# Kernel optimization log

Hardware: AMD Instinct MI355X
Metric: run time of the kernel (lower is better)

Reference implementation:

```python
import jax, jax.numpy as jnp
import numpy as np

EPS = 1e-9
KERNEL = 3


def kernel_tile(x, kernel, stride):
    """im2col-style patch extraction. x: [B,H,W,...] -> [B,OH,OW,kernel*kernel,depth]."""
    B, H, W = x.shape[:3]
    depth = int(np.prod(x.shape[3:]))
    x = x.reshape(B, H, W, depth)
    OH = (H - kernel) // stride + 1
    OW = (W - kernel) // stride + 1
    patches = jnp.stack(
        [x[:, i:i + (OH - 1) * stride + 1:stride, j:j + (OW - 1) * stride + 1:stride, :]
         for i in range(kernel) for j in range(kernel)], axis=3)
    return patches  # [B,OH,OW,k*k,depth]


def em_routing(votes, i_act, beta_v, beta_a, routings):
    # votes: [B,S,S,I,O,16], i_act: [B,S,S,I], beta_*: [1,1,1,O]
    I, O = votes.shape[-3], votes.shape[-2]
    rr = jnp.full((I, O, 1), 1.0 / O, dtype=votes.dtype)
    i_act = i_act[..., None, None]           # [B,S,S,I,1,1]
    bv = beta_v[..., None, :, None]          # [1,1,1,1,O,1]
    ba = beta_a[..., None, :, None]
    it_min, it_max = 1.0, min(float(routings), 3.0)
    o_mean = o_act = None
    for it in range(routings):
        inv_temp = it_min + (it_max - it_min) * it / max(1.0, routings - 1.0)
        # M-step
        rr_prime = rr * i_act                                        # [B,S,S,I,O,1]
        rr_sum = jnp.sum(rr_prime, axis=-3, keepdims=True)           # [B,S,S,1,O,1]
        o_mean = jnp.sum(rr_prime * votes, axis=-3, keepdims=True) / rr_sum  # [B,S,S,1,O,16]
        o_stdv = jnp.sqrt(jnp.sum(rr_prime * jnp.square(votes - o_mean), axis=-3, keepdims=True) / rr_sum)
        o_cost = (bv + jnp.log(o_stdv + EPS)) * rr_sum               # [B,S,S,1,O,16]
        o_act = jax.nn.sigmoid(inv_temp * (ba - jnp.sum(o_cost, axis=-1, keepdims=True)))  # [B,S,S,1,O,1]
        if it < routings - 1:
            # E-step: log Gaussian prob of each vote under each output capsule
            o_p = (-jnp.sum(jnp.square(votes - o_mean) / (2.0 * jnp.square(o_stdv)), axis=-1, keepdims=True)
                   - jnp.sum(jnp.log(o_stdv + EPS), axis=-1, keepdims=True))  # [B,S,S,I,O,1]
            zz = jnp.log(o_act + EPS) + o_p
            rr = jax.nn.softmax(zz, axis=-2)                          # softmax over O
    pose = jnp.squeeze(o_mean, axis=-3)      # [B,S,S,O,16]
    act = jnp.squeeze(o_act, axis=(-3, -1))  # [B,S,S,O]
    return pose, act


def setup_inputs() -> dict:
    key = jax.random.key(0)
    ks = jax.random.split(key, 5)
    B, H, W, I_SIZE, O_SIZE = 4, 14, 14, 32, 32
    inputs_pose = jax.random.normal(ks[0], (B, H, W, I_SIZE, 4, 4), dtype=jnp.float32)
    inputs_activation = jax.random.uniform(ks[1], (B, H, W, I_SIZE), dtype=jnp.float32)
    w = jax.random.normal(ks[2], (1, 3 * 3 * I_SIZE, O_SIZE, 4, 4), dtype=jnp.float32)
    beta_v = 0.1 * jax.random.normal(ks[3], (1, 1, 1, O_SIZE), dtype=jnp.float32)
    beta_a = 0.1 * jax.random.normal(ks[4], (1, 1, 1, O_SIZE), dtype=jnp.float32)
    return {"inputs_pose": inputs_pose, "inputs_activation": inputs_activation,
            "w": w, "beta_v": beta_v, "beta_a": beta_a, "stride": 1, "routings": 3}


def reference(inputs_pose, inputs_activation, w, beta_v, beta_a, stride, routings):
    B = inputs_pose.shape[0]
    pose_size = inputs_pose.shape[-1]            # 4
    i_size = inputs_pose.shape[3]
    o_size = w.shape[2]
    tp = kernel_tile(inputs_pose, KERNEL, stride)        # [B,S,S,9,i*16]
    ta = kernel_tile(inputs_activation, KERNEL, stride)  # [B,S,S,9,i]
    S = ta.shape[1]
    I = KERNEL * KERNEL * i_size
    poses = tp.reshape(-1, I, pose_size, pose_size)      # [N,I,4,4], N = B*S*S
    acts = ta.reshape(B, S, S, I)
    # vote transform: per (input capsule, output capsule) 4x4 matmul
    votes = jnp.einsum('nipq,ioqr->niopr', poses, w[0])  # [N,I,O,4,4]
    votes = votes.reshape(B, S, S, I, o_size, pose_size * pose_size)
    pose, activation = em_routing(votes, acts, beta_v, beta_a, routings)
    pose = pose.reshape(B, S, S, o_size, pose_size, pose_size)
    return pose, activation
```

## Files before the change

### kernel.cpp

```cpp
#include <hip/hip_runtime.h>
#include <math.h>

namespace {

constexpr int SOUT = 12;
constexpr int OCAP = 32;
constexpr int PD   = 16;
constexpr int NI   = 288;
constexpr int SUBS = 4;
constexpr int ISUB = NI / SUBS;
constexpr int NPOS = 4 * SOUT * SOUT;
constexpr float EPSF = 1e-9f;
constexpr int CHUNK = 33 * 32;
constexpr size_t POSE_OUT = (size_t)NPOS * OCAP * PD;

typedef float v2f __attribute__((ext_vector_type(2)));

__device__ __forceinline__ v2f vfma(v2f a, v2f b, v2f c) { return __builtin_elementwise_fma(a, b, c); }
__device__ __forceinline__ v2f splat(float a) { v2f r; r.x = a; r.y = a; return r; }

template<int CTRL>
__device__ __forceinline__ float dppf(float x) {
    return __int_as_float(__builtin_amdgcn_update_dpp(0, __float_as_int(x), CTRL, 0xF, 0xF, true));
}
#define SWZ16(x) __int_as_float(__builtin_amdgcn_ds_swizzle(__float_as_int(x), (16 << 10) | 0x1F))

__device__ __forceinline__ float redmax32(float x) {
    x = fmaxf(x, dppf<0xB1>(x));
    x = fmaxf(x, dppf<0x4E>(x));
    x = fmaxf(x, dppf<0x141>(x));
    x = fmaxf(x, dppf<0x140>(x));
    x = fmaxf(x, SWZ16(x));
    return x;
}
__device__ __forceinline__ float redsum32(float x) {
    x += dppf<0xB1>(x);
    x += dppf<0x4E>(x);
    x += dppf<0x141>(x);
    x += dppf<0x140>(x);
    x += SWZ16(x);
    return x;
}

__device__ __forceinline__ void loadW(const float* __restrict__ p, v2f (&W)[8]) {
    const float4 w0 = *reinterpret_cast<const float4*>(p);
    const float4 w1 = *reinterpret_cast<const float4*>(p + 4);
    const float4 w2 = *reinterpret_cast<const float4*>(p + 8);
    const float4 w3 = *reinterpret_cast<const float4*>(p + 12);
    W[0].x=w0.x; W[0].y=w0.y; W[1].x=w0.z; W[1].y=w0.w;
    W[2].x=w1.x; W[2].y=w1.y; W[3].x=w1.z; W[3].y=w1.w;
    W[4].x=w2.x; W[4].y=w2.y; W[5].x=w2.z; W[5].y=w2.w;
    W[6].x=w3.x; W[6].y=w3.y; W[7].x=w3.z; W[7].y=w3.w;
}

__device__ __forceinline__ void vote8(const float* __restrict__ pr, const v2f (&W)[8], v2f (&v)[8]) {
    #pragma unroll
    for (int p = 0; p < 4; ++p) {
        const float4 pv = *reinterpret_cast<const float4*>(pr + p * 4);
        #pragma unroll
        for (int h = 0; h < 2; ++h) {
            v2f acc = splat(pv.w) * W[6 + h];
            acc = vfma(splat(pv.z), W[4 + h], acc);
            acc = vfma(splat(pv.y), W[2 + h], acc);
            acc = vfma(splat(pv.x), W[0 + h], acc);
            v[p * 2 + h] = acc;
        }
    }
}

__device__ __forceinline__ constexpr int DH(int h) { return (h >> 1) * 4 + (h & 1) * 2; }

template<int SWEEP>
__global__ __launch_bounds__(256, 2)
void sweep_kernel(const float* __restrict__ pose_in,
                  const float* __restrict__ act_in,
                  const float* __restrict__ wmat,
                  const float* __restrict__ beta_v,
                  const float* __restrict__ beta_a,
                  const float* __restrict__ prev,
                  float* __restrict__ outbuf)
{
    __shared__ __align__(16) float sP[ISUB * PD];
    __shared__ float sA[ISUB];
    __shared__ __align__(8) float sStat[OCAP][2 * PD + 2];
    __shared__ float sBias[OCAP];
    __shared__ float sRed[2][33][33];

    const int bid = blockIdx.x;
    const int n   = bid >> 2;
    const int sub = bid & 3;
    const int b   = n / (SOUT * SOUT);
    const int yx  = n % (SOUT * SOUT);
    const int y   = yx / SOUT;
    const int x   = yx % SOUT;

    const int t    = threadIdx.x;
    const int wave = t >> 6;
    const int o    = t & 31;
    const int slot = t >> 5;
    const int half = slot & 1;

    {
        const float4* src = reinterpret_cast<const float4*>(pose_in);
        float4* dst = reinterpret_cast<float4*>(sP);
        for (int u = t; u < ISUB * 4; u += 256) {
            const int il = u >> 2;
            const int i  = sub * ISUB + il;
            const int k = i >> 5, c = i & 31;
            const int ki = k / 3, kj = k - ki * 3;
            const int cell = (b * 14 + y + ki) * 14 + (x + kj);
            dst[u] = src[(size_t)(cell * 32 + c) * 4 + (u & 3)];
        }
        if (t < ISUB) {
            const int i = sub * ISUB + t;
            const int k = i >> 5, c = i & 31;
            const int ki = k / 3, kj = k - ki * 3;
            const int cell = (b * 14 + y + ki) * 14 + (x + kj);
            sA[t] = act_in[(size_t)cell * 32 + c];
        }
    }

    if constexpr (SWEEP > 0) {
        const int oo = t >> 3, dp = t & 7, d0 = dp * 2;
        const float* base = prev + (size_t)n * (SUBS * CHUNK);
        float s0 = 0.f, S1a = 0.f, S1b = 0.f, S2a = 0.f, S2b = 0.f;
        #pragma unroll
        for (int s = 0; s < SUBS; ++s) {
            const float* c = base + s * CHUNK;
            s0  += c[32 * 32 + oo];
            S1a += c[(d0)      * 32 + oo];
            S1b += c[(d0 + 1)  * 32 + oo];
            S2a += c[(16 + d0) * 32 + oo];
            S2b += c[(17 + d0) * 32 + oo];
        }
        const float inv = 1.f / s0;
        const float m0 = S1a * inv, m1 = S1b * inv;
        const float v0 = fmaxf(fmaf(-m0, m0, S2a * inv), 0.f);
        const float v1 = fmaxf(fmaf(-m1, m1, S2b * inv), 0.f);
        const float i20 = 0.5f / fmaxf(v0, 1e-30f);
        const float i21 = 0.5f / fmaxf(v1, 1e-30f);
        float ll = __logf(sqrtf(v0) + EPSF) + __logf(sqrtf(v1) + EPSF);
        float c0 = m0 * m0 * i20 + m1 * m1 * i21;
        sStat[oo][d0]          = i20;
        sStat[oo][d0 + 1]      = i21;
        sStat[oo][16 + d0]     = -2.f * m0 * i20;
        sStat[oo][17 + d0]     = -2.f * m1 * i21;
        #pragma unroll
        for (int m = 1; m <= 4; m <<= 1) {
            ll += __shfl_xor(ll, m, 8);
            c0 += __shfl_xor(c0, m, 8);
        }
        if (dp == 0) {
            const float cost = s0 * fmaf(16.f, beta_v[oo], ll);
            const float oact = 1.f / (1.f + __expf(-(float)SWEEP * (beta_a[oo] - cost)));
            sBias[oo] = __logf(oact + EPSF) - ll - c0;
        }
    }
    __syncthreads();

    float bias_r = 0.f;
    v2f i2r[8], ngr[8];
    if constexpr (SWEEP > 0) {
        bias_r = sBias[o];
        #pragma unroll
        for (int h = 0; h < 8; ++h) {
            i2r[h] = *reinterpret_cast<const v2f*>(&sStat[o][2 * h]);
            ngr[h] = *reinterpret_cast<const v2f*>(&sStat[o][16 + 2 * h]);
        }
    }

    v2f s1[8], s2[8];
    float s0acc = 0.f;
    #pragma unroll
    for (int h = 0; h < 8; ++h) { s1[h] = splat(0.f); s2[h] = splat(0.f); }

    const float* wbase = wmat + ((size_t)(sub * ISUB + slot) * OCAP + o) * PD;

    v2f WA[8], WB[8];
    loadW(wbase, WA);

#define STEP(st, Wc, Wn)                                                   \
    {                                                                      \
        if ((st) < 8) loadW(wbase + (size_t)((st) + 1) * 4096, Wn);        \
        const int il = (st) * 8 + slot;                                    \
        v2f v[8];                                                          \
        vote8(&sP[il * PD], Wc, v);                                        \
        const float a_i = sA[il];                                          \
        float rrp;                                                         \
        if constexpr (SWEEP == 0) {                                        \
            rrp = a_i * (1.0f / 32.0f);                                    \
        } else {                                                           \
            v2f ts2 = splat(0.f);                                          \
            _Pragma("unroll")                                              \
            for (int h = 0; h < 8; ++h) {                                  \
                const v2f tmp = vfma(v[h], i2r[h], ngr[h]);                \
                ts2 = vfma(v[h], tmp, ts2);                                \
            }                                                              \
            const float zz = bias_r - (ts2.x + ts2.y);                     \
            const float m = redmax32(zz);                                  \
            const float e = __expf(zz - m);                                \
            const float es = redsum32(e);                                  \
            rrp = __fdividef(e, es) * a_i;                                 \
        }                                                                  \
        s0acc += rrp;                                                      \
        const v2f rr2 = splat(rrp);                                        \
        _Pragma("unroll")                                                  \
        for (int h = 0; h < 8; ++h) {                                      \
            const v2f rv = rr2 * v[h];                                     \
            s1[h] = s1[h] + rv;                                            \
            s2[h] = vfma(rv, v[h], s2[h]);                                 \
        }                                                                  \
    }

    STEP(0, WA, WB); STEP(1, WB, WA); STEP(2, WA, WB); STEP(3, WB, WA);
    STEP(4, WA, WB); STEP(5, WB, WA); STEP(6, WA, WB); STEP(7, WB, WA);
    STEP(8, WA, WB);
#undef STEP

    #pragma unroll
    for (int h = 0; h < 8; ++h) {
        s1[h].x += __shfl_xor(s1[h].x, 32, 64);
        s1[h].y += __shfl_xor(s1[h].y, 32, 64);
        s2[h].x += __shfl_xor(s2[h].x, 32, 64);
        s2[h].y += __shfl_xor(s2[h].y, 32, 64);
    }
    s0acc += __shfl_xor(s0acc, 32, 64);

    if (wave < 2 && half == 0) {
        #pragma unroll
        for (int h = 0; h < 8; ++h) {
            sRed[wave][DH(h)][o]          = s1[h].x;
            sRed[wave][DH(h) + 1][o]      = s1[h].y;
            sRed[wave][16 + DH(h)][o]     = s2[h].x;
            sRed[wave][16 + DH(h) + 1][o] = s2[h].y;
        }
        sRed[wave][32][o] = s0acc;
    }
    __syncthreads();
    if (wave >= 2 && half == 0) {
        #pragma unroll
        for (int h = 0; h < 8; ++h) {
            sRed[wave - 2][DH(h)][o]          += s1[h].x;
            sRed[wave - 2][DH(h) + 1][o]      += s1[h].y;
            sRed[wave - 2][16 + DH(h)][o]     += s2[h].x;
            sRed[wave - 2][16 + DH(h) + 1][o] += s2[h].y;
        }
        sRed[wave - 2][32][o] += s0acc;
    }
    __syncthreads();

    float* dstc = outbuf + (size_t)bid * CHUNK;
    const int oc = t & 31;
    for (int j = t >> 5; j < 33; j += 8)
        dstc[j * 32 + oc] = sRed[0][j][oc] + sRed[1][j][oc];
}

__global__ __launch_bounds__(256, 4)
void final_kernel(const float* __restrict__ prev,
                  const float* __restrict__ beta_v,
                  const float* __restrict__ beta_a,
                  float* __restrict__ out)
{
    const int n  = blockIdx.x;
    const int t  = threadIdx.x;
    const int oo = t >> 3, dp = t & 7, d0 = dp * 2;
    const float* base = prev + (size_t)n * (SUBS * CHUNK);
    float s0 = 0.f, S1a = 0.f, S1b = 0.f, S2a = 0.f, S2b = 0.f;
    #pragma unroll
    for (int s = 0; s < SUBS; ++s) {
        const float* c = base + s * CHUNK;
        s0  += c[32 * 32 + oo];
        S1a += c[(d0)      * 32 + oo];
        S1b += c[(d0 + 1)  * 32 + oo];
        S2a += c[(16 + d0) * 32 + oo];
        S2b += c[(17 + d0) * 32 + oo];
    }
    const float inv = 1.f / s0;
    const float m0 = S1a * inv, m1 = S1b * inv;
    out[(size_t)n * (OCAP * PD) + oo * PD + d0]     = m0;
    out[(size_t)n * (OCAP * PD) + oo * PD + d0 + 1] = m1;

    const float v0 = fmaxf(fmaf(-m0, m0, S2a * inv), 0.f);
    const float v1 = fmaxf(fmaf(-m1, m1, S2b * inv), 0.f);
    float lt = __logf(sqrtf(v0) + EPSF) + __logf(sqrtf(v1) + EPSF);
    lt += __shfl_xor(lt, 1, 8);
    lt += __shfl_xor(lt, 2, 8);
    lt += __shfl_xor(lt, 4, 8);
    if (dp == 0) {
        const float cost = s0 * fmaf(16.f, beta_v[oo], lt);
        const float oact = 1.f / (1.f + __expf(-3.0f * (beta_a[oo] - cost)));
        out[POSE_OUT + (size_t)n * OCAP + oo] = oact;
    }
}

}

extern "C" void kernel_launch(void* const* d_in, const int* in_sizes, int n_in,
                              void* d_out, int out_size, void* d_ws, size_t ws_size,
                              hipStream_t stream) {
    const float* pose_in = (const float*)d_in[0];
    const float* act_in  = (const float*)d_in[1];
    const float* wmat    = (const float*)d_in[2];
    const float* beta_v  = (const float*)d_in[3];
    const float* beta_a  = (const float*)d_in[4];
    float* out = (float*)d_out;

    float* bufA = (float*)d_ws;
    float* bufB = bufA + (size_t)NPOS * SUBS * CHUNK;

    dim3 block(256);
    dim3 gridS(NPOS * SUBS);
    dim3 gridF(NPOS);

    sweep_kernel<0><<<gridS, block, 0, stream>>>(pose_in, act_in, wmat, beta_v, beta_a, nullptr, bufA);
    sweep_kernel<1><<<gridS, block, 0, stream>>>(pose_in, act_in, wmat, beta_v, beta_a, bufA, bufB);
    sweep_kernel<2><<<gridS, block, 0, stream>>>(pose_in, act_in, wmat, beta_v, beta_a, bufB, bufA);
    final_kernel<<<gridF, block, 0, stream>>>(bufA, beta_v, beta_a, out);
}
```

Measured before the change: 117.7 us.

## Share weight loads across batch in sweep blocks and split stats into separate kernel

Each sweep block now covers one spatial position and input sub-range for all four batch elements, one wave per batch. Every wave walks the same weight sequence, so weight traffic is shared through cache. The per-output mean and variance statistics move into a separate stats kernel that writes to a global buffer, and the cross-wave shared-memory reduction is dropped in favour of direct per-wave writes. The cost is a quarter as many blocks with longer serial loops per thread, plus two extra kernel launches.

After: 126.2 us. 1.07x slower.

```diff
diff --git a/kernel.cpp b/kernel.cpp
--- a/kernel.cpp
+++ b/kernel.cpp
@@ -12,6 +12,7 @@
 constexpr int NPOS = 4 * SOUT * SOUT;
 constexpr float EPSF = 1e-9f;
 constexpr int CHUNK = 33 * 32;
+constexpr int SSTR  = 36;
 constexpr size_t POSE_OUT = (size_t)NPOS * OCAP * PD;
 
 typedef float v2f __attribute__((ext_vector_type(2)));
@@ -75,98 +76,64 @@
 void sweep_kernel(const float* __restrict__ pose_in,
                   const float* __restrict__ act_in,
                   const float* __restrict__ wmat,
-                  const float* __restrict__ beta_v,
-                  const float* __restrict__ beta_a,
-                  const float* __restrict__ prev,
+                  const float* __restrict__ statbuf,
                   float* __restrict__ outbuf)
 {
-    __shared__ __align__(16) float sP[ISUB * PD];
-    __shared__ float sA[ISUB];
-    __shared__ __align__(8) float sStat[OCAP][2 * PD + 2];
-    __shared__ float sBias[OCAP];
-    __shared__ float sRed[2][33][33];
+    __shared__ __align__(16) float sP[4 * ISUB * PD];
+    __shared__ float sA[4 * ISUB];
 
     const int bid = blockIdx.x;
-    const int n   = bid >> 2;
+    const int yx  = bid >> 2;
     const int sub = bid & 3;
-    const int b   = n / (SOUT * SOUT);
-    const int yx  = n % (SOUT * SOUT);
     const int y   = yx / SOUT;
     const int x   = yx % SOUT;
 
     const int t    = threadIdx.x;
     const int wave = t >> 6;
-    const int o    = t & 31;
-    const int slot = t >> 5;
-    const int half = slot & 1;
+    const int lane = t & 63;
+    const int o    = lane & 31;
+    const int half = lane >> 5;
 
     {
         const float4* src = reinterpret_cast<const float4*>(pose_in);
         float4* dst = reinterpret_cast<float4*>(sP);
-        for (int u = t; u < ISUB * 4; u += 256) {
-            const int il = u >> 2;
-            const int i  = sub * ISUB + il;
-            const int k = i >> 5, c = i & 31;
+        for (int u = t; u < 4 * ISUB * 4; u += 256) {
+            const int bs   = u / (ISUB * 4);
+            const int r    = u - bs * (ISUB * 4);
+            const int il   = r >> 2;
+            const int comp = r & 3;
+            const int ig   = sub * ISUB + il;
+            const int k = ig >> 5, c = ig & 31;
             const int ki = k / 3, kj = k - ki * 3;
-            const int cell = (b * 14 + y + ki) * 14 + (x + kj);
-            dst[u] = src[(size_t)(cell * 32 + c) * 4 + (u & 3)];
-        }
-        if (t < ISUB) {
-            const int i = sub * ISUB + t;
-            const int k = i >> 5, c = i & 31;
+            const int cell = (bs * 14 + y + ki) * 14 + (x + kj);
+            dst[u] = src[(size_t)(cell * 32 + c) * 4 + comp];
+        }
+        for (int u = t; u < 4 * ISUB; u += 256) {
+            const int bs = u / ISUB;
+            const int il = u - bs * ISUB;
+            const int ig = sub * ISUB + il;
+            const int k = ig >> 5, c = ig & 31;
             const int ki = k / 3, kj = k - ki * 3;
-            const int cell = (b * 14 + y + ki) * 14 + (x + kj);
-            sA[t] = act_in[(size_t)cell * 32 + c];
-        }
-    }
-
-    if constexpr (SWEEP > 0) {
-        const int oo = t >> 3, dp = t & 7, d0 = dp * 2;
-        const float* base = prev + (size_t)n * (SUBS * CHUNK);
-        float s0 = 0.f, S1a = 0.f, S1b = 0.f, S2a = 0.f, S2b = 0.f;
-        #pragma unroll
-        for (int s = 0; s < SUBS; ++s) {
-            const float* c = base + s * CHUNK;
-            s0  += c[32 * 32 + oo];
-            S1a += c[(d0)      * 32 + oo];
-            S1b += c[(d0 + 1)  * 32 + oo];
-            S2a += c[(16 + d0) * 32 + oo];
-            S2b += c[(17 + d0) * 32 + oo];
-        }
-        const float inv = 1.f / s0;
-        const float m0 = S1a * inv, m1 = S1b * inv;
-        const float v0 = fmaxf(fmaf(-m0, m0, S2a * inv), 0.f);
-        const float v1 = fmaxf(fmaf(-m1, m1, S2b * inv), 0.f);
-        const float i20 = 0.5f / fmaxf(v0, 1e-30f);
-        const float i21 = 0.5f / fmaxf(v1, 1e-30f);
-        float ll = __logf(sqrtf(v0) + EPSF) + __logf(sqrtf(v1) + EPSF);
-        float c0 = m0 * m0 * i20 + m1 * m1 * i21;
-        sStat[oo][d0]          = i20;
-        sStat[oo][d0 + 1]      = i21;
-        sStat[oo][16 + d0]     = -2.f * m0 * i20;
-        sStat[oo][17 + d0]     = -2.f * m1 * i21;
-        #pragma unroll
-        for (int m = 1; m <= 4; m <<= 1) {
-            ll += __shfl_xor(ll, m, 8);
-            c0 += __shfl_xor(c0, m, 8);
-        }
-        if (dp == 0) {
-            const float cost = s0 * fmaf(16.f, beta_v[oo], ll);
-            const float oact = 1.f / (1.f + __expf(-(float)SWEEP * (beta_a[oo] - cost)));
-            sBias[oo] = __logf(oact + EPSF) - ll - c0;
+            const int cell = (bs * 14 + y + ki) * 14 + (x + kj);
+            sA[u] = act_in[(size_t)cell * 32 + c];
         }
     }
     __syncthreads();
+
+    const int n = wave * (SOUT * SOUT) + yx;
 
     float bias_r = 0.f;
     v2f i2r[8], ngr[8];
     if constexpr (SWEEP > 0) {
-        bias_r = sBias[o];
+        const float* st = statbuf + ((size_t)n * OCAP + o) * SSTR;
         #pragma unroll
-        for (int h = 0; h < 8; ++h) {
-            i2r[h] = *reinterpret_cast<const v2f*>(&sStat[o][2 * h]);
-            ngr[h] = *reinterpret_cast<const v2f*>(&sStat[o][16 + 2 * h]);
-        }
+        for (int q = 0; q < 4; ++q) {
+            const float4 a = *reinterpret_cast<const float4*>(st + q * 4);
+            i2r[q*2].x = a.x; i2r[q*2].y = a.y; i2r[q*2+1].x = a.z; i2r[q*2+1].y = a.w;
+            const float4 g = *reinterpret_cast<const float4*>(st + 16 + q * 4);
+            ngr[q*2].x = g.x; ngr[q*2].y = g.y; ngr[q*2+1].x = g.z; ngr[q*2+1].y = g.w;
+        }
+        bias_r = st[32];
     }
 
     v2f s1[8], s2[8];
@@ -174,18 +141,20 @@
     #pragma unroll
     for (int h = 0; h < 8; ++h) { s1[h] = splat(0.f); s2[h] = splat(0.f); }
 
-    const float* wbase = wmat + ((size_t)(sub * ISUB + slot) * OCAP + o) * PD;
+    const float* wth = wmat + ((size_t)((sub * ISUB + half) * OCAP) + o) * PD;
+    const float* pbase = sP + wave * ISUB * PD;
+    const float* abase = sA + wave * ISUB;
 
     v2f WA[8], WB[8];
-    loadW(wbase, WA);
-
-#define STEP(st, Wc, Wn)                                                   \
+    loadW(wth, WA);
+
+#define STEP(st_, Wc, Wn)                                                  \
     {                                                                      \
-        if ((st) < 8) loadW(wbase + (size_t)((st) + 1) * 4096, Wn);        \
-        const int il = (st) * 8 + slot;                                    \
+        if ((st_) < 35) loadW(wth + (size_t)((st_) + 1) * 1024, Wn);       \
+        const int il = (st_) * 2 + half;                                   \
         v2f v[8];                                                          \
-        vote8(&sP[il * PD], Wc, v);                                        \
-        const float a_i = sA[il];                                          \
+        vote8(pbase + il * PD, Wc, v);                                     \
+        const float a_i = abase[il];                                       \
         float rrp;                                                         \
         if constexpr (SWEEP == 0) {                                        \
             rrp = a_i * (1.0f / 32.0f);                                    \
@@ -212,9 +181,11 @@
         }                                                                  \
     }
 
-    STEP(0, WA, WB); STEP(1, WB, WA); STEP(2, WA, WB); STEP(3, WB, WA);
-    STEP(4, WA, WB); STEP(5, WB, WA); STEP(6, WA, WB); STEP(7, WB, WA);
-    STEP(8, WA, WB);
+    #pragma unroll 1
+    for (int kk = 0; kk < 18; ++kk) {
+        STEP(2 * kk,     WA, WB);
+        STEP(2 * kk + 1, WB, WA);
+    }
 #undef STEP
 
     #pragma unroll
@@ -226,33 +197,65 @@
     }
     s0acc += __shfl_xor(s0acc, 32, 64);
 
-    if (wave < 2 && half == 0) {
+    if (half == 0) {
+        float* dstc = outbuf + (size_t)(n * SUBS + sub) * CHUNK;
         #pragma unroll
         for (int h = 0; h < 8; ++h) {
-            sRed[wave][DH(h)][o]          = s1[h].x;
-            sRed[wave][DH(h) + 1][o]      = s1[h].y;
-            sRed[wave][16 + DH(h)][o]     = s2[h].x;
-            sRed[wave][16 + DH(h) + 1][o] = s2[h].y;
-        }
-        sRed[wave][32][o] = s0acc;
-    }
-    __syncthreads();
-    if (wave >= 2 && half == 0) {
-        #pragma unroll
-        for (int h = 0; h < 8; ++h) {
-            sRed[wave - 2][DH(h)][o]          += s1[h].x;
-            sRed[wave - 2][DH(h) + 1][o]      += s1[h].y;
-            sRed[wave - 2][16 + DH(h)][o]     += s2[h].x;
-            sRed[wave - 2][16 + DH(h) + 1][o] += s2[h].y;
-        }
-        sRed[wave - 2][32][o] += s0acc;
-    }
-    __syncthreads();
-
-    float* dstc = outbuf + (size_t)bid * CHUNK;
-    const int oc = t & 31;
-    for (int j = t >> 5; j < 33; j += 8)
-        dstc[j * 32 + oc] = sRed[0][j][oc] + sRed[1][j][oc];
+            dstc[DH(h) * 32 + o]          = s1[h].x;
+            dstc[(DH(h) + 1) * 32 + o]    = s1[h].y;
+            dstc[(16 + DH(h)) * 32 + o]   = s2[h].x;
+            dstc[(17 + DH(h)) * 32 + o]   = s2[h].y;
+        }
+        dstc[32 * 32 + o] = s0acc;
+    }
+}
+
+template<int IT>
+__global__ __launch_bounds__(256, 4)
+void stats_kernel(const float* __restrict__ prev,
+                  const float* __restrict__ beta_v,
+                  const float* __restrict__ beta_a,
+                  float* __restrict__ statbuf)
+{
+    const int n  = blockIdx.x;
+    const int t  = threadIdx.x;
+    const int oo = t >> 3, dp = t & 7, d0 = dp * 2;
+    const float* base = prev + (size_t)n * (SUBS * CHUNK);
+    float s0 = 0.f, S1a = 0.f, S1b = 0.f, S2a = 0.f, S2b = 0.f;
+    #pragma unroll
+    for (int s = 0; s < SUBS; ++s) {
+        const float* c = base + s * CHUNK;
+        s0  += c[32 * 32 + oo];
+        S1a += c[(d0)      * 32 + oo];
+        S1b += c[(d0 + 1)  * 32 + oo];
+        S2a += c[(16 + d0) * 32 + oo];
+        S2b += c[(17 + d0) * 32 + oo];
+    }
+    const float inv = 1.f / s0;
+    const float m0 = S1a * inv, m1 = S1b * inv;
+    const float v0 = fmaxf(fmaf(-m0, m0, S2a * inv), 0.f);
+    const float v1 = fmaxf(fmaf(-m1, m1, S2b * inv), 0.f);
+    const float i20 = 0.5f / fmaxf(v0, 1e-30f);
+    const float i21 = 0.5f / fmaxf(v1, 1e-30f);
+    float ll = __logf(sqrtf(v0) + EPSF) + __logf(sqrtf(v1) + EPSF);
+    float c0 = m0 * m0 * i20 + m1 * m1 * i21;
+
+    float* st = statbuf + ((size_t)n * OCAP + oo) * SSTR;
+    st[d0]          = i20;
+    st[d0 + 1]      = i21;
+    st[16 + d0]     = -2.f * m0 * i20;
+    st[17 + d0]     = -2.f * m1 * i21;
+
+    #pragma unroll
+    for (int m = 1; m <= 4; m <<= 1) {
+        ll += __shfl_xor(ll, m, 8);
+        c0 += __shfl_xor(c0, m, 8);
+    }
+    if (dp == 0) {
+        const float cost = s0 * fmaf(16.f, beta_v[oo], ll);
+        const float oact = 1.f / (1.f + __expf(-(float)IT * (beta_a[oo] - cost)));
+        st[32] = __logf(oact + EPSF) - ll - c0;
+    }
 }
 
 __global__ __launch_bounds__(256, 4)
@@ -305,15 +308,18 @@
     const float* beta_a  = (const float*)d_in[4];
     float* out = (float*)d_out;
 
-    float* bufA = (float*)d_ws;
-    float* bufB = bufA + (size_t)NPOS * SUBS * CHUNK;
+    float* bufA    = (float*)d_ws;
+    float* bufB    = bufA + (size_t)NPOS * SUBS * CHUNK;
+    float* statbuf = bufB + (size_t)NPOS * SUBS * CHUNK;
 
     dim3 block(256);
-    dim3 gridS(NPOS * SUBS);
-    dim3 gridF(NPOS);
-
-    sweep_kernel<0><<<gridS, block, 0, stream>>>(pose_in, act_in, wmat, beta_v, beta_a, nullptr, bufA);
-    sweep_kernel<1><<<gridS, block, 0, stream>>>(pose_in, act_in, wmat, beta_v, beta_a, bufA, bufB);
-    sweep_kernel<2><<<gridS, block, 0, stream>>>(pose_in, act_in, wmat, beta_v, beta_a, bufB, bufA);
-    final_kernel<<<gridF, block, 0, stream>>>(bufA, beta_v, beta_a, out);
-}
+    dim3 gridS(NPOS);
+    dim3 gridN(NPOS);
+
+    sweep_kernel<0><<<gridS, block, 0, stream>>>(pose_in, act_in, wmat, nullptr, bufA);
+    stats_kernel<1><<<gridN, block, 0, stream>>>(bufA, beta_v, beta_a, statbuf);
+    sweep_kernel<1><<<gridS, block, 0, stream>>>(pose_in, act_in, wmat, statbuf, bufB);
+    stats_kernel<2><<<gridN, block, 0, stream>>>(bufB, beta_v, beta_a, statbuf);
+    sweep_kernel<2><<<gridS, block, 0, stream>>>(pose_in, act_in, wmat, statbuf, bufA);
+    final_kernel<<<gridN, block, 0, stream>>>(bufA, beta_v, beta_a, out);
+}
```
